# Kernel optimization log

Measured on AMD Instinct MI355X. Metric: run time of the kernel, lower is better.

Reference implementation:

```python
import jax, jax.numpy as jnp
import numpy as np

D_MODEL = 1024
N_HEADS = 16
HEAD_DIM = D_MODEL // N_HEADS


def setup_inputs() -> dict:
    key = jax.random.key(0)
    ks = jax.random.split(key, 9)
    B, L = 2, 2048
    s = 1.0 / np.sqrt(D_MODEL)
    return {
        "x": jax.random.normal(ks[0], (B, L, D_MODEL), dtype=jnp.float32),
        "q_w": jax.random.normal(ks[1], (D_MODEL, D_MODEL), dtype=jnp.float32) * s,
        "q_b": jnp.zeros((D_MODEL,), dtype=jnp.float32),
        "k_w": jax.random.normal(ks[2], (D_MODEL, D_MODEL), dtype=jnp.float32) * s,
        "k_b": jnp.zeros((D_MODEL,), dtype=jnp.float32),
        "v_w": jax.random.normal(ks[3], (D_MODEL, D_MODEL), dtype=jnp.float32) * s,
        "v_b": jnp.zeros((D_MODEL,), dtype=jnp.float32),
        "o_w": jax.random.normal(ks[4], (D_MODEL, D_MODEL), dtype=jnp.float32) * s,
        "o_b": jnp.zeros((D_MODEL,), dtype=jnp.float32),
    }


def _rope_tables(L, dtype):
    # inv_freq: [head_dim//2]
    inv_freq = 1.0 / (10000.0 ** (jnp.arange(0, HEAD_DIM, 2, dtype=dtype) / HEAD_DIM))
    t = jnp.arange(L, dtype=dtype)
    freqs = t[:, None] * inv_freq[None, :]          # [L, hd/2]
    emb = jnp.concatenate([freqs, freqs], axis=-1)  # [L, hd]
    return jnp.cos(emb), jnp.sin(emb)


def _rotate_half(x):
    x1, x2 = x[..., : HEAD_DIM // 2], x[..., HEAD_DIM // 2 :]
    return jnp.concatenate([-x2, x1], axis=-1)


def reference(x, q_w, q_b, k_w, k_b, v_w, v_b, o_w, o_b):
    B, L, D = x.shape
    H, hd = N_HEADS, HEAD_DIM
    # Linear (torch: x @ W.T + b), then split heads -> [B, H, L, hd]
    def proj(w, b):
        y = jnp.einsum("bld,ed->ble", x, w) + b
        return y.reshape(B, L, H, hd).transpose(0, 2, 1, 3)

    q, k, v = proj(q_w, q_b), proj(k_w, k_b), proj(v_w, v_b)

    cos, sin = _rope_tables(L, x.dtype)  # [L, hd] each, broadcast over B,H
    q = q * cos + _rotate_half(q) * sin
    k = k * cos + _rotate_half(k) * sin

    scores = jnp.einsum("bhqd,bhkd->bhqk", q, k) / jnp.sqrt(jnp.asarray(hd, x.dtype))
    attn = jax.nn.softmax(scores, axis=-1)
    out = jnp.einsum("bhqk,bhkd->bhqd", attn, v)
    out = out.transpose(0, 2, 1, 3).reshape(B, L, D)
    return jnp.einsum("bld,ed->ble", out, o_w) + o_b
```

## Files before the change

### kernel.cpp

```cpp
#include <hip/hip_runtime.h>
#include <math.h>

#define SEQ   2048
#define NH    16
#define HD    64
#define DM    1024
#define BATCH 2
#define MROWS (BATCH*SEQ)

typedef __attribute__((ext_vector_type(8))) short short8;
typedef __attribute__((ext_vector_type(4))) float f32x4;
typedef __attribute__((ext_vector_type(16))) float f32x16;
typedef unsigned short ushort;
typedef unsigned int uint;

__device__ __forceinline__ ushort f2bf(float x){
  unsigned int u = __float_as_uint(x);
  unsigned int r = (u + 0x7fffu + ((u>>16)&1u)) >> 16;
  return (ushort)r;
}
__device__ __forceinline__ void gload16(const ushort* g, ushort* l){
  __builtin_amdgcn_global_load_lds(
      (const __attribute__((address_space(1))) unsigned int*)(g),
      (__attribute__((address_space(3))) unsigned int*)(l), 16, 0, 0);
}

__global__ void rope_tables_kernel(float* __restrict__ cosT, float* __restrict__ sinT){
  int idx = blockIdx.x*blockDim.x + threadIdx.x;
  if (idx >= SEQ*32) return;
  int i = idx & 31, l = idx >> 5;
  float e = (float)(2*i) / 64.0f;
  float inv = 1.0f / powf(10000.0f, e);
  float ang = (float)l * inv;
  cosT[idx] = cosf(ang);
  sinT[idx] = sinf(ang);
}

__global__ void cast_all_kernel(
    const float* __restrict__ X,
    const float* __restrict__ wq, const float* __restrict__ wk,
    const float* __restrict__ wv, const float* __restrict__ wo,
    ushort* __restrict__ Xh,
    ushort* __restrict__ hq, ushort* __restrict__ hk,
    ushort* __restrict__ hv, ushort* __restrict__ ho)
{
  int idx = blockIdx.x*blockDim.x + threadIdx.x;
  const float* src; ushort* dh; int off;
  const int NX = (MROWS*DM) >> 2;
  if (idx < NX){ src = X; dh = Xh; off = idx; }
  else {
    int t = idx - NX;
    int sel = t >> 18;
    off = t & 262143;
    src = sel==0 ? wq : sel==1 ? wk : sel==2 ? wv : wo;
    dh  = sel==0 ? hq : sel==1 ? hk : sel==2 ? hv : ho;
  }
  float4 v = ((const float4*)src)[off];
  uint2 hp;
  hp.x = (unsigned)f2bf(v.x) | ((unsigned)f2bf(v.y)<<16);
  hp.y = (unsigned)f2bf(v.z) | ((unsigned)f2bf(v.w)<<16);
  ((uint2*)dh)[off] = hp;
}

__global__ __launch_bounds__(256) void gemm_qkv_mfma(
    const ushort* __restrict__ Xh,
    const ushort* __restrict__ Whq, const ushort* __restrict__ Whk, const ushort* __restrict__ Whv,
    const float* __restrict__ bq, const float* __restrict__ bk, const float* __restrict__ bv,
    const float* __restrict__ cosT, const float* __restrict__ sinT,
    ushort* __restrict__ Qb, ushort* __restrict__ Kb, ushort* __restrict__ Vb)
{
  __shared__ __align__(16) ushort Ls[2][128*64];
  ushort* As = Ls[0];
  ushort* Bs = Ls[1];
  const int tid = threadIdx.x, w = tid>>6, lane = tid&63;
  const int c = lane & 15, g = lane >> 4;
  const int wr = w >> 1, wc = w & 1;
  const int m0   = blockIdx.x * 128;
  const int ncat = blockIdx.y * 128;
  const int which = ncat >> 10;
  const int n0    = ncat & 1023;
  const ushort* Bhi = which==0 ? Whq : which==1 ? Whk : Whv;
  const float*  bias= which==0 ? bq  : which==1 ? bk  : bv;

  const int srow = lane >> 3;
  const int scol = ((lane & 7) ^ srow) << 3;

  f32x4 acc[4][4] = {};
  for (int k0 = 0; k0 < DM; k0 += 64){
    __syncthreads();
    #pragma unroll
    for (int i=0;i<4;i++){
      const int rb = w*32 + i*8;
      gload16(Xh  + (size_t)(m0 + rb + srow)*DM + k0 + scol, &As[rb*64]);
      gload16(Bhi + (size_t)(n0 + rb + srow)*DM + k0 + scol, &Bs[rb*64]);
    }
    __syncthreads();
    #pragma unroll
    for (int kc=0;kc<2;kc++){
      short8 a[4], b[4];
      #pragma unroll
      for (int m=0;m<4;m++){
        int row = wr*64 + m*16 + c;
        a[m] = *(const short8*)&As[row*64 + ((((kc<<2)+g) ^ (row&7))<<3)];
      }
      #pragma unroll
      for (int n=0;n<4;n++){
        int row = wc*64 + n*16 + c;
        b[n] = *(const short8*)&Bs[row*64 + ((((kc<<2)+g) ^ (row&7))<<3)];
      }
      #pragma unroll
      for (int m=0;m<4;m++)
        #pragma unroll
        for (int n=0;n<4;n++)
          acc[m][n] = __builtin_amdgcn_mfma_f32_16x16x32_bf16(a[m], b[n], acc[m][n], 0,0,0);
    }
  }

  const int hh = (n0 + wc*64) >> 6;
  if (which == 0){
    #pragma unroll
    for (int m=0;m<4;m++){
      #pragma unroll
      for (int r=0;r<4;r++){
        int mrow = m0 + wr*64 + m*16 + 4*g + r;
        int bb = mrow >> 11, l = mrow & (SEQ-1);
        size_t obase = (((size_t)bb*NH + hh)*SEQ + l)*HD;
        #pragma unroll
        for (int n=0;n<2;n++){
          int d1 = n*16 + c, d2 = d1 + 32;
          float v1 = acc[m][n  ][r] + bias[hh*64 + d1];
          float v2 = acc[m][n+2][r] + bias[hh*64 + d2];
          float co = cosT[l*32 + d1], si = sinT[l*32 + d1];
          Qb[obase + d1] = f2bf((v1*co - v2*si)*0.125f);
          Qb[obase + d2] = f2bf((v2*co + v1*si)*0.125f);
        }
      }
    }
  } else {
    __syncthreads();
    ushort* L0 = Ls[0];
    const int base = (wc*2 + wr)*4096;
    #pragma unroll
    for (int m=0;m<4;m++){
      const int kbl = (m>>1)&1;
      #pragma unroll
      for (int r=0;r<4;r++){
        const int l31 = (m&1)*16 + 4*g + r;
        int mrow = m0 + wr*64 + m*16 + 4*g + r;
        int l = mrow & (SEQ-1);
        #pragma unroll
        for (int n=0;n<2;n++){
          int d1 = n*16 + c, d2 = d1 + 32;
          float v1 = acc[m][n  ][r] + bias[hh*64 + d1];
          float v2 = acc[m][n+2][r] + bias[hh*64 + d2];
          if (which == 1){
            float co = cosT[l*32 + d1], si = sinT[l*32 + d1];
            float o1 = v1*co - v2*si;
            float o2 = v2*co + v1*si;
            L0[base + (kbl*4 + n    )*512 + (l31 + 32*(c>>3))*8 + (c&7)] = f2bf(o1);
            L0[base + (kbl*4 + n + 2)*512 + (l31 + 32*(c>>3))*8 + (c&7)] = f2bf(o2);
          } else {
            int pos = ((n*16 + c) + 32*(g>>1))*8 + 4*(g&1) + r;
            L0[base + (    kbl*2 + (m&1))*512 + pos] = f2bf(v1);
            L0[base + (4 + kbl*2 + (m&1))*512 + pos] = f2bf(v2);
          }
        }
      }
    }
    __syncthreads();
    ushort* Out = (which==1) ? Kb : Vb;
    const int head2 = (n0 + (w>>1)*64) >> 6;
    const int ltile = ((m0 & (SEQ-1)) >> 6) + (w & 1);
    const int bb    = m0 >> 11;
    ushort* dst = Out + (((size_t)bb*NH + head2)*(SEQ/64) + ltile)*4096;
    const ushort* srcl = L0 + w*4096;
    #pragma unroll
    for (int i=0;i<8;i++)
      *(short8*)(dst + i*512 + lane*8) = *(const short8*)(srcl + i*512 + lane*8);
  }
}

__global__ __launch_bounds__(256) void flash_mfma_kernel(
    const ushort* __restrict__ Qb, const ushort* __restrict__ Kb,
    const ushort* __restrict__ Vb, ushort* __restrict__ AOh)
{
  __shared__ __align__(16) ushort Ks[2][8][512];
  __shared__ __align__(16) ushort Vs[2][8][512];

  const int tid  = threadIdx.x;
  const int w    = tid >> 6;
  const int lane = tid & 63;
  const int c    = lane & 31;
  const int h    = lane >> 5;

  const int hw = blockIdx.x;
  const int lg = (hw & 7)*64 + (hw >> 3);
  const int bx = lg & 15, hd = (lg >> 4) & 15, b = lg >> 8;
  const int bh = b*NH + hd;
  const int q0 = bx*128 + w*32;

  const ushort* Kimg = Kb + (size_t)bh*SEQ*HD;
  const ushort* Vimg = Vb + (size_t)bh*SEQ*HD;

  const ushort* Qrow = Qb + ((size_t)bh*SEQ + q0 + c)*HD + 8*h;
  short8 qf[4];
  #pragma unroll
  for (int kc=0;kc<4;kc++) qf[kc] = *(const short8*)(Qrow + kc*16);

  short8 ones;
  #pragma unroll
  for (int i=0;i<8;i++) ones[i] = (short)0x3F80;

  f32x16 oacc[2] = {};
  f32x16 sacc = {};

  #define STAGE(bf, t0) { \
    _Pragma("unroll") for (int i_=0;i_<2;i_++){ \
      int n_ = 2*w + i_; \
      gload16(Kimg + ((t0)>>6)*4096 + n_*512 + lane*8, &Ks[bf][n_][0]); \
      gload16(Vimg + ((t0)>>6)*4096 + n_*512 + lane*8, &Vs[bf][n_][0]); \
    } }

  STAGE(0, 0)
  __syncthreads();

  int buf = 0;
  for (int t0 = 0; t0 < SEQ; t0 += 64){
    if (t0 + 64 < SEQ){
      STAGE(buf ^ 1, t0 + 64)
    }

    #pragma unroll
    for (int kb=0; kb<2; kb++){
      f32x16 s = {};
      __builtin_amdgcn_s_setprio(1);
      #pragma unroll
      for (int kc=0;kc<4;kc++){
        short8 kf = *(const short8*)&Ks[buf][kb*4+kc][lane*8];
        s = __builtin_amdgcn_mfma_f32_32x32x16_bf16(kf, qf[kc], s, 0,0,0);
      }
      __builtin_amdgcn_s_setprio(0);

      uint pk[8];
      #pragma unroll
      for (int i=0;i<8;i++){
        float p0 = __expf(s[2*i]);
        float p1 = __expf(s[2*i+1]);
        asm("v_cvt_pk_bf16_f32 %0, %1, %2" : "=v"(pk[i]) : "v"(p0), "v"(p1));
      }
      asm volatile("v_permlane32_swap_b32 %0, %1" : "+v"(pk[0]), "+v"(pk[2]));
      asm volatile("v_permlane32_swap_b32 %0, %1" : "+v"(pk[1]), "+v"(pk[3]));
      asm volatile("v_permlane32_swap_b32 %0, %1" : "+v"(pk[4]), "+v"(pk[6]));
      asm volatile("v_permlane32_swap_b32 %0, %1" : "+v"(pk[5]), "+v"(pk[7]));
      short8 pa0, pa1;
      ((uint*)&pa0)[0]=pk[0]; ((uint*)&pa0)[1]=pk[1]; ((uint*)&pa0)[2]=pk[2]; ((uint*)&pa0)[3]=pk[3];
      ((uint*)&pa1)[0]=pk[4]; ((uint*)&pa1)[1]=pk[5]; ((uint*)&pa1)[2]=pk[6]; ((uint*)&pa1)[3]=pk[7];

      __builtin_amdgcn_s_setprio(1);
      #pragma unroll
      for (int db=0; db<2; db++){
        short8 v0 = *(const short8*)&Vs[buf][db*4 + kb*2 + 0][lane*8];
        short8 v1 = *(const short8*)&Vs[buf][db*4 + kb*2 + 1][lane*8];
        oacc[db] = __builtin_amdgcn_mfma_f32_32x32x16_bf16(pa0, v0, oacc[db], 0,0,0);
        oacc[db] = __builtin_amdgcn_mfma_f32_32x32x16_bf16(pa1, v1, oacc[db], 0,0,0);
      }
      sacc = __builtin_amdgcn_mfma_f32_32x32x16_bf16(pa0, ones, sacc, 0,0,0);
      sacc = __builtin_amdgcn_mfma_f32_32x32x16_bf16(pa1, ones, sacc, 0,0,0);
      __builtin_amdgcn_s_setprio(0);
    }

    __syncthreads();
    buf ^= 1;
  }
  #undef STAGE

  float inv[16];
  #pragma unroll
  for (int r=0;r<16;r++) inv[r] = 1.0f / sacc[r];
  #pragma unroll
  for (int db=0; db<2; db++){
    #pragma unroll
    for (int r=0;r<16;r++){
      int q = q0 + (r&3) + 8*(r>>2) + 4*h;
      AOh[((size_t)b*SEQ + q)*DM + hd*HD + db*32 + c] = f2bf(oacc[db][r] * inv[r]);
    }
  }
}

__global__ __launch_bounds__(256) void gemm_o_mfma(
    const ushort* __restrict__ AOh, const ushort* __restrict__ Who,
    const float* __restrict__ bo, float* __restrict__ Y)
{
  __shared__ __align__(16) ushort As[128*64];
  __shared__ __align__(16) ushort Bs[128*64];
  const int tid = threadIdx.x, w = tid>>6, lane = tid&63;
  const int c = lane & 15, g = lane >> 4;
  const int wr = w >> 1, wc = w & 1;
  const int m0 = blockIdx.x * 128;
  const int n0 = blockIdx.y * 128;

  const int srow = lane >> 3;
  const int scol = ((lane & 7) ^ srow) << 3;

  f32x4 acc[4][4] = {};
  for (int k0 = 0; k0 < DM; k0 += 64){
    __syncthreads();
    #pragma unroll
    for (int i=0;i<4;i++){
      const int rb = w*32 + i*8;
      gload16(AOh + (size_t)(m0 + rb + srow)*DM + k0 + scol, &As[rb*64]);
      gload16(Who + (size_t)(n0 + rb + srow)*DM + k0 + scol, &Bs[rb*64]);
    }
    __syncthreads();
    #pragma unroll
    for (int kc=0;kc<2;kc++){
      short8 a[4], b[4];
      #pragma unroll
      for (int m=0;m<4;m++){
        int row = wr*64 + m*16 + c;
        a[m] = *(const short8*)&As[row*64 + ((((kc<<2)+g) ^ (row&7))<<3)];
      }
      #pragma unroll
      for (int n=0;n<4;n++){
        int row = wc*64 + n*16 + c;
        b[n] = *(const short8*)&Bs[row*64 + ((((kc<<2)+g) ^ (row&7))<<3)];
      }
      #pragma unroll
      for (int m=0;m<4;m++)
        #pragma unroll
        for (int n=0;n<4;n++)
          acc[m][n] = __builtin_amdgcn_mfma_f32_16x16x32_bf16(a[m], b[n], acc[m][n], 0,0,0);
    }
  }

  #pragma unroll
  for (int m=0;m<4;m++){
    #pragma unroll
    for (int r=0;r<4;r++){
      int mrow = m0 + wr*64 + m*16 + 4*g + r;
      #pragma unroll
      for (int n=0;n<4;n++){
        int ncol = n0 + wc*64 + n*16 + c;
        Y[(size_t)mrow*DM + ncol] = acc[m][n][r] + bo[ncol];
      }
    }
  }
}

extern "C" void kernel_launch(void* const* d_in, const int* in_sizes, int n_in,
                              void* d_out, int out_size, void* d_ws, size_t ws_size,
                              hipStream_t stream)
{
  const float* x  = (const float*)d_in[0];
  const float* qw = (const float*)d_in[1];
  const float* qb = (const float*)d_in[2];
  const float* kw = (const float*)d_in[3];
  const float* kb = (const float*)d_in[4];
  const float* vw = (const float*)d_in[5];
  const float* vb = (const float*)d_in[6];
  const float* ow = (const float*)d_in[7];
  const float* ob = (const float*)d_in[8];
  float* out = (float*)d_out;

  const size_t NE = (size_t)MROWS*DM;
  const size_t WE = (size_t)DM*DM;
  float* cosT = (float*)d_ws;
  float* sinT = cosT + SEQ*32;
  ushort* p = (ushort*)(sinT + SEQ*32);
  ushort* Xh  = p;            p += NE;
  ushort* Whq = p;            p += WE;
  ushort* Whk = p;            p += WE;
  ushort* Whv = p;            p += WE;
  ushort* Who = p;            p += WE;
  ushort* Qb  = p;            p += NE;
  ushort* Kb  = p;            p += NE;
  ushort* Vb  = p;            p += NE;
  ushort* AOh = p;            p += NE;

  hipLaunchKernelGGL(rope_tables_kernel, dim3((SEQ*32+255)/256), dim3(256), 0, stream, cosT, sinT);
  hipLaunchKernelGGL(cast_all_kernel, dim3((NE/4 + WE)/256), dim3(256), 0, stream,
                     x, qw, kw, vw, ow, Xh, Whq, Whk, Whv, Who);
  hipLaunchKernelGGL(gemm_qkv_mfma, dim3(MROWS/128, 3072/128), dim3(256), 0, stream,
                     Xh, Whq, Whk, Whv, qb, kb, vb, cosT, sinT, Qb, Kb, Vb);
  hipLaunchKernelGGL(flash_mfma_kernel, dim3(512), dim3(256), 0, stream,
                     Qb, Kb, Vb, AOh);
  hipLaunchKernelGGL(gemm_o_mfma, dim3(MROWS/128, DM/128), dim3(256), 0, stream,
                     AOh, Who, ob, out);
}
```

Baseline: 132.2 us.

## Split flash attention KV range in two halves with combine kernel

Splits the attention KV sequence into two halves so twice as many blocks (1024) run the flash kernel. Each writes unnormalized bf16 partial outputs and row sums, and a new combine kernel adds them and normalizes into AOh. This targets low occupancy with only 512 blocks on many CUs. In exchange it adds an extra launch, extra global traffic for partial outputs, and an extra bf16 rounding of partial sums. It relies on no running max being used, so the two halves combine by simple addition.

```diff
diff --git a/kernel.cpp b/kernel.cpp
--- a/kernel.cpp
+++ b/kernel.cpp
@@ -18,6 +18,9 @@
   unsigned int u = __float_as_uint(x);
   unsigned int r = (u + 0x7fffu + ((u>>16)&1u)) >> 16;
   return (ushort)r;
+}
+__device__ __forceinline__ float bf2f(ushort h){
+  return __uint_as_float(((unsigned int)h) << 16);
 }
 __device__ __forceinline__ void gload16(const ushort* g, ushort* l){
   __builtin_amdgcn_global_load_lds(
@@ -182,7 +185,7 @@
 
 __global__ __launch_bounds__(256) void flash_mfma_kernel(
     const ushort* __restrict__ Qb, const ushort* __restrict__ Kb,
-    const ushort* __restrict__ Vb, ushort* __restrict__ AOh)
+    const ushort* __restrict__ Vb, ushort* __restrict__ Opart, float* __restrict__ Ssum)
 {
   __shared__ __align__(16) ushort Ks[2][8][512];
   __shared__ __align__(16) ushort Vs[2][8][512];
@@ -194,10 +197,11 @@
   const int h    = lane >> 5;
 
   const int hw = blockIdx.x;
-  const int lg = (hw & 7)*64 + (hw >> 3);
-  const int bx = lg & 15, hd = (lg >> 4) & 15, b = lg >> 8;
+  const int lg = (hw & 7)*128 + (hw >> 3);
+  const int bx = lg & 15, hd = (lg >> 4) & 15, b = (lg >> 8) & 1, half = lg >> 9;
   const int bh = b*NH + hd;
   const int q0 = bx*128 + w*32;
+  const int t0base = half*(SEQ/2);
 
   const ushort* Kimg = Kb + (size_t)bh*SEQ*HD;
   const ushort* Vimg = Vb + (size_t)bh*SEQ*HD;
@@ -221,12 +225,13 @@
       gload16(Vimg + ((t0)>>6)*4096 + n_*512 + lane*8, &Vs[bf][n_][0]); \
     } }
 
-  STAGE(0, 0)
+  STAGE(0, t0base)
   __syncthreads();
 
   int buf = 0;
-  for (int t0 = 0; t0 < SEQ; t0 += 64){
-    if (t0 + 64 < SEQ){
+  for (int t = 0; t < SEQ/2; t += 64){
+    const int t0 = t0base + t;
+    if (t + 64 < SEQ/2){
       STAGE(buf ^ 1, t0 + 64)
     }
 
@@ -274,17 +279,44 @@
   }
   #undef STAGE
 
-  float inv[16];
-  #pragma unroll
-  for (int r=0;r<16;r++) inv[r] = 1.0f / sacc[r];
+  ushort* Op = Opart + (size_t)half*MROWS*DM;
   #pragma unroll
   for (int db=0; db<2; db++){
     #pragma unroll
     for (int r=0;r<16;r++){
       int q = q0 + (r&3) + 8*(r>>2) + 4*h;
-      AOh[((size_t)b*SEQ + q)*DM + hd*HD + db*32 + c] = f2bf(oacc[db][r] * inv[r]);
-    }
-  }
+      Op[((size_t)b*SEQ + q)*DM + hd*HD + db*32 + c] = f2bf(oacc[db][r]);
+    }
+  }
+  if (c == 0){
+    float* Sp = Ssum + (size_t)half*BATCH*NH*SEQ + ((size_t)b*NH + hd)*SEQ;
+    #pragma unroll
+    for (int r=0;r<16;r++){
+      int q = q0 + (r&3) + 8*(r>>2) + 4*h;
+      Sp[q] = sacc[r];
+    }
+  }
+}
+
+__global__ void combine_kernel(const ushort* __restrict__ Opart, const float* __restrict__ Ssum,
+                               ushort* __restrict__ AOh)
+{
+  const size_t NE = (size_t)MROWS*DM;
+  int i = blockIdx.x*blockDim.x + threadIdx.x;
+  size_t e = (size_t)i*8;
+  int d = (int)(e & (DM-1));
+  int q = (int)((e >> 10) & (SEQ-1));
+  int b = (int)(e >> 21);
+  int hh = d >> 6;
+  size_t sidx = ((size_t)b*NH + hh)*SEQ + q;
+  float inv = 1.0f / (Ssum[sidx] + Ssum[(size_t)BATCH*NH*SEQ + sidx]);
+  short8 a = *(const short8*)(Opart + e);
+  short8 bb = *(const short8*)(Opart + NE + e);
+  short8 o;
+  #pragma unroll
+  for (int j=0;j<8;j++)
+    o[j] = (short)f2bf((bf2f((ushort)a[j]) + bf2f((ushort)bb[j]))*inv);
+  *(short8*)(AOh + e) = o;
 }
 
 __global__ __launch_bounds__(256) void gemm_o_mfma(
@@ -366,7 +398,8 @@
   const size_t WE = (size_t)DM*DM;
   float* cosT = (float*)d_ws;
   float* sinT = cosT + SEQ*32;
-  ushort* p = (ushort*)(sinT + SEQ*32);
+  float* Ssum = sinT + SEQ*32;
+  ushort* p = (ushort*)(Ssum + 2*BATCH*NH*SEQ);
   ushort* Xh  = p;            p += NE;
   ushort* Whq = p;            p += WE;
   ushort* Whk = p;            p += WE;
@@ -375,6 +408,7 @@
   ushort* Qb  = p;            p += NE;
   ushort* Kb  = p;            p += NE;
   ushort* Vb  = p;            p += NE;
+  ushort* Opart = p;          p += 2*NE;
   ushort* AOh = p;            p += NE;
 
   hipLaunchKernelGGL(rope_tables_kernel, dim3((SEQ*32+255)/256), dim3(256), 0, stream, cosT, sinT);
@@ -382,8 +416,10 @@
                      x, qw, kw, vw, ow, Xh, Whq, Whk, Whv, Who);
   hipLaunchKernelGGL(gemm_qkv_mfma, dim3(MROWS/128, 3072/128), dim3(256), 0, stream,
                      Xh, Whq, Whk, Whv, qb, kb, vb, cosT, sinT, Qb, Kb, Vb);
-  hipLaunchKernelGGL(flash_mfma_kernel, dim3(512), dim3(256), 0, stream,
-                     Qb, Kb, Vb, AOh);
+  hipLaunchKernelGGL(flash_mfma_kernel, dim3(1024), dim3(256), 0, stream,
+                     Qb, Kb, Vb, Opart, Ssum);
+  hipLaunchKernelGGL(combine_kernel, dim3(MROWS*DM/8/256), dim3(256), 0, stream,
+                     Opart, Ssum, AOh);
   hipLaunchKernelGGL(gemm_o_mfma, dim3(MROWS/128, DM/128), dim3(256), 0, stream,
                      AOh, Who, ob, out);
 }
```

Result: slower. 139.9 us (+5.8%).
